# Kernel tuning notes

Measured on AMD Instinct MI355X. Metric: run time of the kernel, lower is better.

The kernel has to match this reference:

```python
import jax, jax.numpy as jnp
import numpy as np

V, D, H, L, F, S_MAX = 32000, 1024, 16, 4, 4096, 1024
DK = D // H
EPS = 1e-5


def pos_encoding(S, Dm):
    pos = jnp.arange(S, dtype=jnp.float32)[:, None]
    div = jnp.exp(jnp.arange(0, Dm, 2, dtype=jnp.float32) * (-jnp.log(10000.0) / Dm))
    ang = pos * div  # [S, D/2]
    return jnp.stack([jnp.sin(ang), jnp.cos(ang)], axis=-1).reshape(S, Dm)


def layernorm(x, g, b):
    mu = jnp.mean(x, axis=-1, keepdims=True)
    var = jnp.mean(jnp.square(x - mu), axis=-1, keepdims=True)
    return (x - mu) * jax.lax.rsqrt(var + EPS) * g + b


def setup_inputs() -> dict:
    key = jax.random.key(0)
    ks = jax.random.split(key, 20)
    s = 0.02
    B, S = 4, 1024
    x = jax.random.randint(ks[0], (B, S), 1, V)  # avoid pad token 0
    return {
        'x': x,
        'emb': jax.random.normal(ks[1], (V, D), jnp.float32) * s,
        'Wq': jax.random.normal(ks[2], (L, D, D), jnp.float32) * s,
        'Wk': jax.random.normal(ks[3], (L, D, D), jnp.float32) * s,
        'Wv': jax.random.normal(ks[4], (L, D, D), jnp.float32) * s,
        'Wo': jax.random.normal(ks[5], (L, D, D), jnp.float32) * s,
        'bo': jnp.zeros((L, D), jnp.float32),
        'ln1_g': jnp.ones((L, D), jnp.float32),
        'ln1_b': jnp.zeros((L, D), jnp.float32),
        'ln2_g': jnp.ones((L, D), jnp.float32),
        'ln2_b': jnp.zeros((L, D), jnp.float32),
        'W1': jax.random.normal(ks[6], (L, D, F), jnp.float32) * s,
        'b1': jnp.zeros((L, F), jnp.float32),
        'W2': jax.random.normal(ks[7], (L, F, D), jnp.float32) * s,
        'b2': jnp.zeros((L, D), jnp.float32),
        'Wout': jax.random.normal(ks[8], (D, V), jnp.float32) * s,
        'bout': jnp.zeros((V,), jnp.float32),
    }


def reference(x, emb, Wq, Wk, Wv, Wo, bo, ln1_g, ln1_b, ln2_g, ln2_b, W1, b1, W2, b2, Wout, bout):
    B, S = x.shape
    # mask: padding (key tokens != 0) AND causal, shape [B, 1, S, S]
    pad = (x != 0)[:, None, None, :]
    causal = jnp.tril(jnp.ones((S, S), bool))[None, None]
    mask = pad & causal

    h = emb[x] * jnp.sqrt(jnp.float32(D)) + pos_encoding(S, D)[None]

    scale = jnp.sqrt(jnp.float32(DK))
    for l in range(L):
        q = (h @ Wq[l]).reshape(B, S, H, DK).transpose(0, 2, 1, 3)
        k = (h @ Wk[l]).reshape(B, S, H, DK).transpose(0, 2, 1, 3)
        v = (h @ Wv[l]).reshape(B, S, H, DK).transpose(0, 2, 1, 3)
        scores = jnp.einsum('bhqd,bhkd->bhqk', q, k) / scale
        scores = jnp.where(mask, scores, -jnp.inf)
        attn = jax.nn.softmax(scores, axis=-1)
        ctx = jnp.einsum('bhqk,bhkd->bhqd', attn, v)
        ctx = ctx.transpose(0, 2, 1, 3).reshape(B, S, D)
        attn_out = ctx @ Wo[l] + bo[l]
        h = layernorm(h + attn_out, ln1_g[l], ln1_b[l])
        ff = jax.nn.gelu(h @ W1[l] + b1[l], approximate=False) @ W2[l] + b2[l]
        h = layernorm(h + ff, ln2_g[l], ln2_b[l])

    return h @ Wout + bout
```

## Files before the change

### kernel.cpp

```cpp
#include <hip/hip_runtime.h>
#include <hip/hip_bf16.h>
#include <math.h>

constexpr int Bc = 4, Sc = 1024, Dc = 1024, Hc = 16, Lc = 4, Fc = 4096, Vc = 32000;
constexpr int DKc = 64;
constexpr int Mc = Bc * Sc;
constexpr float EPSc = 1e-5f;

typedef __attribute__((ext_vector_type(8))) short short8v;
typedef __attribute__((ext_vector_type(4))) float f32x4;

__device__ __forceinline__ ushort bf16_rne(float f) {
    uint u = __float_as_uint(f);
    return (ushort)((u + 0x7fffu + ((u >> 16) & 1u)) >> 16);
}
__device__ __forceinline__ void split2(float f, ushort& h, ushort& l) {
    ushort hh = bf16_rne(f);
    float hf = __uint_as_float(((uint)hh) << 16);
    h = hh;
    l = bf16_rne(f - hf);
}

__global__ __launch_bounds__(256) void embed_k(const int* __restrict__ x,
                                               const float* __restrict__ emb,
                                               float* __restrict__ h) {
    int m = blockIdx.x;
    int s = m & (Sc - 1);
    int tid = threadIdx.x;
    int d0 = tid * 4;
    int tok = x[m];
    float4 e = *(const float4*)&emb[(size_t)tok * Dc + d0];
    const float c = -9.210340371976184f / 512.0f;
    float p0 = (float)(tid * 2);
    float fs = (float)s;
    float ang0 = fs * __expf(c * p0);
    float ang1 = fs * __expf(c * (p0 + 1.0f));
    float4 o;
    o.x = e.x * 32.0f + sinf(ang0);
    o.y = e.y * 32.0f + cosf(ang0);
    o.z = e.z * 32.0f + sinf(ang1);
    o.w = e.w * 32.0f + cosf(ang1);
    *(float4*)&h[(size_t)m * Dc + d0] = o;
}

__device__ __forceinline__ float gelu_exact(float v) {
    return 0.5f * v * (1.0f + erff(v * 0.70710678118654752f));
}

__global__ __launch_bounds__(256) void wconv_k(const float* __restrict__ W,
                                               ushort* __restrict__ hi,
                                               ushort* __restrict__ lo,
                                               int Kd, int Nd) {
    __shared__ float T[64][65];
    int nt = blockIdx.x * 64, kt = blockIdx.y * 64;
    int tid = threadIdx.x;
    int r16 = tid >> 4, c4 = (tid & 15) * 4;
#pragma unroll
    for (int p = 0; p < 4; p++) {
        int k = r16 + p * 16;
        float4 v = *(const float4*)&W[(size_t)(kt + k) * Nd + nt + c4];
        T[k][c4 + 0] = v.x; T[k][c4 + 1] = v.y;
        T[k][c4 + 2] = v.z; T[k][c4 + 3] = v.w;
    }
    __syncthreads();
#pragma unroll
    for (int p = 0; p < 4; p++) {
        int n = r16 + p * 16;
        ushort4 oh, ol;
        ushort hv, lv;
        split2(T[c4 + 0][n], hv, lv); oh.x = hv; ol.x = lv;
        split2(T[c4 + 1][n], hv, lv); oh.y = hv; ol.y = lv;
        split2(T[c4 + 2][n], hv, lv); oh.z = hv; ol.z = lv;
        split2(T[c4 + 3][n], hv, lv); oh.w = hv; ol.w = lv;
        size_t o = (size_t)(nt + n) * Kd + kt + c4;
        *(ushort4*)&hi[o] = oh;
        *(ushort4*)&lo[o] = ol;
    }
}

template<int MODE>
__global__ __launch_bounds__(256) void mgemm_k(const float* __restrict__ A,
                                               const ushort* __restrict__ Bh_g,
                                               const ushort* __restrict__ Bl_g,
                                               const float* __restrict__ bias,
                                               float* __restrict__ C,
                                               int Kd, int Nd) {
    __shared__ ushort Ah[128][40], Al[128][40], Bh[128][40], Bl[128][40];
    int tid = threadIdx.x;
    int bm = blockIdx.y * 128, bn = blockIdx.x * 128;
    int lane = tid & 63, w = tid >> 6;
    int wr = w >> 1, wc = w & 1;
    int l15 = lane & 15, loct = lane >> 4;

    int sr = tid >> 1, sh = tid & 1;
    const float*  Ap  = A    + (size_t)(bm + sr) * Kd + sh * 16;
    const ushort* Bhp = Bh_g + (size_t)(bn + sr) * Kd + sh * 16;
    const ushort* Blp = Bl_g + (size_t)(bn + sr) * Kd + sh * 16;

    f32x4 acc[4][4];
#pragma unroll
    for (int i = 0; i < 4; i++)
#pragma unroll
        for (int j = 0; j < 4; j++) acc[i][j] = (f32x4){0.f, 0.f, 0.f, 0.f};

    for (int k0 = 0; k0 < Kd; k0 += 32) {
        float4 a0 = *(const float4*)(Ap + k0 + 0);
        float4 a1 = *(const float4*)(Ap + k0 + 4);
        float4 a2 = *(const float4*)(Ap + k0 + 8);
        float4 a3 = *(const float4*)(Ap + k0 + 12);
        uint4 b0 = *(const uint4*)(Bhp + k0);
        uint4 b1 = *(const uint4*)(Bhp + k0 + 8);
        uint4 b2 = *(const uint4*)(Blp + k0);
        uint4 b3 = *(const uint4*)(Blp + k0 + 8);

        union { ushort u[16]; short8v v[2]; } hA, lA;
        float fa[16] = {a0.x, a0.y, a0.z, a0.w, a1.x, a1.y, a1.z, a1.w,
                        a2.x, a2.y, a2.z, a2.w, a3.x, a3.y, a3.z, a3.w};
#pragma unroll
        for (int i = 0; i < 16; i++) {
            ushort hv, lv;
            split2(fa[i], hv, lv);
            hA.u[i] = hv; lA.u[i] = lv;
        }

        __syncthreads();
        *(short8v*)&Ah[sr][sh * 16 + 0] = hA.v[0];
        *(short8v*)&Ah[sr][sh * 16 + 8] = hA.v[1];
        *(short8v*)&Al[sr][sh * 16 + 0] = lA.v[0];
        *(short8v*)&Al[sr][sh * 16 + 8] = lA.v[1];
        *(uint4*)&Bh[sr][sh * 16 + 0] = b0;
        *(uint4*)&Bh[sr][sh * 16 + 8] = b1;
        *(uint4*)&Bl[sr][sh * 16 + 0] = b2;
        *(uint4*)&Bl[sr][sh * 16 + 8] = b3;
        __syncthreads();

        short8v ah[4], al[4], bh[4], bl[4];
#pragma unroll
        for (int m = 0; m < 4; m++) {
            int r = wr * 64 + m * 16 + l15;
            ah[m] = *(const short8v*)&Ah[r][loct * 8];
            al[m] = *(const short8v*)&Al[r][loct * 8];
        }
#pragma unroll
        for (int n = 0; n < 4; n++) {
            int ccol = wc * 64 + n * 16 + l15;
            bh[n] = *(const short8v*)&Bh[ccol][loct * 8];
            bl[n] = *(const short8v*)&Bl[ccol][loct * 8];
        }
#pragma unroll
        for (int m = 0; m < 4; m++)
#pragma unroll
            for (int n = 0; n < 4; n++) {
                acc[m][n] = __builtin_amdgcn_mfma_f32_16x16x32_bf16(ah[m], bh[n], acc[m][n], 0, 0, 0);
                acc[m][n] = __builtin_amdgcn_mfma_f32_16x16x32_bf16(ah[m], bl[n], acc[m][n], 0, 0, 0);
                acc[m][n] = __builtin_amdgcn_mfma_f32_16x16x32_bf16(al[m], bh[n], acc[m][n], 0, 0, 0);
            }
    }

#pragma unroll
    for (int m = 0; m < 4; m++) {
#pragma unroll
        for (int n = 0; n < 4; n++) {
            int gn = bn + wc * 64 + n * 16 + l15;
            float bv = (MODE == 1 || MODE == 2) ? bias[gn] : 0.0f;
#pragma unroll
            for (int j = 0; j < 4; j++) {
                int gm = bm + wr * 64 + m * 16 + loct * 4 + j;
                float v = acc[m][n][j];
                if (MODE == 1 || MODE == 2) v += bv;
                if (MODE == 2) v = gelu_exact(v);
                if (MODE == 3) {
                    int b = gm >> 10, s = gm & 1023;
                    int hh = gn >> 6, dk = gn & 63;
                    C[(((size_t)(b * Hc + hh) * Sc) + s) * DKc + dk] = v;
                } else {
                    C[(size_t)gm * Nd + gn] = v;
                }
            }
        }
    }
}

template<int MODE>
__global__ __launch_bounds__(256) void gemm_k(const float* __restrict__ A,
                                              const float* __restrict__ Bm,
                                              const float* __restrict__ bias,
                                              float* __restrict__ C,
                                              int Kd, int Nd) {
    __shared__ float As[16][68];
    __shared__ float Bs[16][68];
    int tid = threadIdx.x;
    int bm = blockIdx.y * 64;
    int bn = blockIdx.x * 64;
    int tx = tid & 15;
    int ty = tid >> 4;
    float acc[4][4] = {};

    int arow = tid >> 2;
    int akq  = tid & 3;
    int bkrow = tid >> 4;
    int bn4   = tid & 15;

    const float* Aptr = A + (size_t)(bm + arow) * Kd + akq * 4;
    const float* Bptr = Bm + (size_t)bkrow * Nd + bn + bn4 * 4;

    for (int k0 = 0; k0 < Kd; k0 += 16) {
        float4 av = *(const float4*)(Aptr + k0);
        float4 bv = *(const float4*)(Bptr + (size_t)k0 * Nd);
        As[akq * 4 + 0][arow] = av.x;
        As[akq * 4 + 1][arow] = av.y;
        As[akq * 4 + 2][arow] = av.z;
        As[akq * 4 + 3][arow] = av.w;
        *(float4*)&Bs[bkrow][bn4 * 4] = bv;
        __syncthreads();
#pragma unroll
        for (int kk = 0; kk < 16; kk++) {
            float4 a4 = *(const float4*)&As[kk][ty * 4];
            float4 b4 = *(const float4*)&Bs[kk][tx * 4];
            acc[0][0] += a4.x * b4.x; acc[0][1] += a4.x * b4.y;
            acc[0][2] += a4.x * b4.z; acc[0][3] += a4.x * b4.w;
            acc[1][0] += a4.y * b4.x; acc[1][1] += a4.y * b4.y;
            acc[1][2] += a4.y * b4.z; acc[1][3] += a4.y * b4.w;
            acc[2][0] += a4.z * b4.x; acc[2][1] += a4.z * b4.y;
            acc[2][2] += a4.z * b4.z; acc[2][3] += a4.z * b4.w;
            acc[3][0] += a4.w * b4.x; acc[3][1] += a4.w * b4.y;
            acc[3][2] += a4.w * b4.z; acc[3][3] += a4.w * b4.w;
        }
        __syncthreads();
    }

#pragma unroll
    for (int i = 0; i < 4; i++) {
        int gm = bm + ty * 4 + i;
#pragma unroll
        for (int j = 0; j < 4; j++) {
            int gn = bn + tx * 4 + j;
            float v = acc[i][j];
            if (MODE == 1 || MODE == 2) v += bias[gn];
            if (MODE == 2) v = gelu_exact(v);
            C[(size_t)gm * Nd + gn] = v;
        }
    }
}

constexpr int QT = 64;
constexpr int KT = 32;

__global__ __launch_bounds__(64) void fattn_k(const float* __restrict__ Q,
                                              const float* __restrict__ K,
                                              const float* __restrict__ V,
                                              const int* __restrict__ x,
                                              float* __restrict__ ctx) {
    int qt = blockIdx.x;
    int bh = blockIdx.y;
    int b = bh >> 4;
    int hh = bh & 15;
    int tid = threadIdx.x;
    int q = qt * QT + tid;

    __shared__ float Ks[KT][64];
    __shared__ float Vs[KT][64];
    __shared__ int   xs[KT];

    const float* Kb = K + (size_t)bh * Sc * DKc;
    const float* Vb = V + (size_t)bh * Sc * DKc;

    float4 q4[16];
    const float* qp = Q + ((size_t)bh * Sc + q) * DKc;
#pragma unroll
    for (int i = 0; i < 16; i++) q4[i] = *(const float4*)(qp + 4 * i);

    float4 acc[16];
#pragma unroll
    for (int i = 0; i < 16; i++) acc[i] = make_float4(0.f, 0.f, 0.f, 0.f);
    float m = -INFINITY, l = 0.0f;

    int ktiles = (qt * QT + QT) / KT;
    for (int t = 0; t < ktiles; t++) {
        int k0 = t * KT;
        __syncthreads();
        for (int f = tid; f < KT * 16; f += 64) {
            int kr = f >> 4;
            int dc = (f & 15) * 4;
            *(float4*)&Ks[kr][dc] = *(const float4*)&Kb[(size_t)(k0 + kr) * DKc + dc];
            *(float4*)&Vs[kr][dc] = *(const float4*)&Vb[(size_t)(k0 + kr) * DKc + dc];
        }
        if (tid < KT) xs[tid] = x[b * Sc + k0 + tid];
        __syncthreads();

        float sc[KT];
#pragma unroll
        for (int k = 0; k < KT; k++) {
            float4 s4 = make_float4(0.f, 0.f, 0.f, 0.f);
#pragma unroll
            for (int i = 0; i < 16; i++) {
                float4 kv = *(const float4*)&Ks[k][4 * i];
                s4.x += q4[i].x * kv.x;
                s4.y += q4[i].y * kv.y;
                s4.z += q4[i].z * kv.z;
                s4.w += q4[i].w * kv.w;
            }
            float s = (s4.x + s4.y) + (s4.z + s4.w);
            bool valid = ((k0 + k) <= q) && (xs[k] != 0);
            sc[k] = valid ? s * 0.125f : -INFINITY;
        }

        float tm = sc[0];
#pragma unroll
        for (int k = 1; k < KT; k++) tm = fmaxf(tm, sc[k]);
        float mnew = fmaxf(m, tm);
        float corr = __expf(m - mnew);
        l *= corr;
#pragma unroll
        for (int i = 0; i < 16; i++) {
            acc[i].x *= corr; acc[i].y *= corr;
            acc[i].z *= corr; acc[i].w *= corr;
        }
        m = mnew;

#pragma unroll
        for (int k = 0; k < KT; k++) {
            float p = __expf(sc[k] - m);
            l += p;
#pragma unroll
            for (int i = 0; i < 16; i++) {
                float4 vv = *(const float4*)&Vs[k][4 * i];
                acc[i].x += p * vv.x;
                acc[i].y += p * vv.y;
                acc[i].z += p * vv.z;
                acc[i].w += p * vv.w;
            }
        }
    }

    float inv = 1.0f / l;
    float* op = ctx + ((size_t)b * Sc + q) * Dc + hh * 64;
#pragma unroll
    for (int i = 0; i < 16; i++) {
        float4 o;
        o.x = acc[i].x * inv; o.y = acc[i].y * inv;
        o.z = acc[i].z * inv; o.w = acc[i].w * inv;
        *(float4*)(op + 4 * i) = o;
    }
}

__global__ __launch_bounds__(256) void lnadd_k(const float* x, const float* r,
                                               const float* __restrict__ g,
                                               const float* __restrict__ bb,
                                               float* out) {
    int row = blockIdx.x, tid = threadIdx.x;
    int lane = tid & 63, wid = tid >> 6;
    __shared__ float red[8];
    size_t base = (size_t)row * Dc + tid * 4;
    float4 xv = *(const float4*)(x + base);
    float4 rv = *(const float4*)(r + base);
    float v0 = xv.x + rv.x, v1 = xv.y + rv.y, v2 = xv.z + rv.z, v3 = xv.w + rv.w;
    float sum = v0 + v1 + v2 + v3;
    float sq = v0 * v0 + v1 * v1 + v2 * v2 + v3 * v3;
    for (int off = 32; off; off >>= 1) {
        sum += __shfl_down(sum, off);
        sq  += __shfl_down(sq, off);
    }
    if (lane == 0) { red[wid] = sum; red[4 + wid] = sq; }
    __syncthreads();
    if (tid == 0) {
        red[0] = red[0] + red[1] + red[2] + red[3];
        red[4] = red[4] + red[5] + red[6] + red[7];
    }
    __syncthreads();
    float mu = red[0] * (1.0f / Dc);
    float var = red[4] * (1.0f / Dc) - mu * mu;
    float rs = rsqrtf(var + EPSc);
    int d = tid * 4;
    float4 gv = *(const float4*)(g + d);
    float4 bv = *(const float4*)(bb + d);
    float4 o;
    o.x = (v0 - mu) * rs * gv.x + bv.x;
    o.y = (v1 - mu) * rs * gv.y + bv.y;
    o.z = (v2 - mu) * rs * gv.z + bv.z;
    o.w = (v3 - mu) * rs * gv.w + bv.w;
    *(float4*)(out + base) = o;
}

extern "C" void kernel_launch(void* const* d_in, const int* in_sizes, int n_in,
                              void* d_out, int out_size, void* d_ws, size_t ws_size,
                              hipStream_t stream) {
    const int*   x     = (const int*)d_in[0];
    const float* emb   = (const float*)d_in[1];
    const float* Wq    = (const float*)d_in[2];
    const float* Wk    = (const float*)d_in[3];
    const float* Wv    = (const float*)d_in[4];
    const float* Wo    = (const float*)d_in[5];
    const float* bo    = (const float*)d_in[6];
    const float* ln1g  = (const float*)d_in[7];
    const float* ln1b  = (const float*)d_in[8];
    const float* ln2g  = (const float*)d_in[9];
    const float* ln2b  = (const float*)d_in[10];
    const float* W1    = (const float*)d_in[11];
    const float* b1    = (const float*)d_in[12];
    const float* W2    = (const float*)d_in[13];
    const float* b2    = (const float*)d_in[14];
    const float* Wout  = (const float*)d_in[15];
    const float* bout  = (const float*)d_in[16];
    float* out = (float*)d_out;
    float* ws = (float*)d_ws;

    const size_t MD = (size_t)Mc * Dc;
    float* h    = ws;
    float* q    = ws + 1 * MD;
    float* k    = ws + 2 * MD;
    float* v    = ws + 3 * MD;
    float* ctx  = ws + 4 * MD;
    float* tmp  = ws + 5 * MD;
    float* ff1  = q;

    const size_t DD = (size_t)Dc * Dc;
    const size_t DF = (size_t)Dc * Fc;
    const size_t PL = 8 * DD + 4 * DF;
    ushort* conv = (ushort*)out;

    const size_t used  = 6 * MD * sizeof(float);
    const size_t woutE = (size_t)Dc * Vc;
    bool wout_mfma = ws_size >= used + 2 * woutE * sizeof(ushort);
    ushort* woc_h = (ushort*)((char*)ws + used);
    ushort* woc_l = woc_h + woutE;

    embed_k<<<Mc, 256, 0, stream>>>(x, emb, h);

    for (int l = 0; l < Lc; l++) {
        ushort* base = conv + (size_t)l * PL;
        wconv_k<<<dim3(16, 16), 256, 0, stream>>>(Wq + (size_t)l * DD, base + 0 * DD, base + 1 * DD, Dc, Dc);
        wconv_k<<<dim3(16, 16), 256, 0, stream>>>(Wk + (size_t)l * DD, base + 2 * DD, base + 3 * DD, Dc, Dc);
        wconv_k<<<dim3(16, 16), 256, 0, stream>>>(Wv + (size_t)l * DD, base + 4 * DD, base + 5 * DD, Dc, Dc);
        wconv_k<<<dim3(16, 16), 256, 0, stream>>>(Wo + (size_t)l * DD, base + 6 * DD, base + 7 * DD, Dc, Dc);
        wconv_k<<<dim3(64, 16), 256, 0, stream>>>(W1 + (size_t)l * DF, base + 8 * DD, base + 8 * DD + DF, Dc, Fc);
        wconv_k<<<dim3(16, 64), 256, 0, stream>>>(W2 + (size_t)l * DF, base + 8 * DD + 2 * DF, base + 8 * DD + 3 * DF, Fc, Dc);
    }
    if (wout_mfma)
        wconv_k<<<dim3(Vc / 64, 16), 256, 0, stream>>>(Wout, woc_h, woc_l, Dc, Vc);

    dim3 g1(Dc / 128, Mc / 128);
    dim3 gF(Fc / 128, Mc / 128);
    dim3 gV(Vc / 128, Mc / 128);

    for (int l = 0; l < Lc; l++) {
        ushort* base = conv + (size_t)l * PL;

        mgemm_k<3><<<g1, 256, 0, stream>>>(h, base + 0 * DD, base + 1 * DD, nullptr, q, Dc, Dc);
        mgemm_k<3><<<g1, 256, 0, stream>>>(h, base + 2 * DD, base + 3 * DD, nullptr, k, Dc, Dc);
        mgemm_k<3><<<g1, 256, 0, stream>>>(h, base + 4 * DD, base + 5 * DD, nullptr, v, Dc, Dc);

        fattn_k<<<dim3(Sc / QT, Bc * Hc), QT, 0, stream>>>(q, k, v, x, ctx);

        mgemm_k<1><<<g1, 256, 0, stream>>>(ctx, base + 6 * DD, base + 7 * DD, bo + l * Dc, tmp, Dc, Dc);
        lnadd_k<<<Mc, 256, 0, stream>>>(h, tmp, ln1g + l * Dc, ln1b + l * Dc, h);

        mgemm_k<2><<<gF, 256, 0, stream>>>(h, base + 8 * DD, base + 8 * DD + DF, b1 + l * Fc, ff1, Dc, Fc);
        mgemm_k<1><<<g1, 256, 0, stream>>>(ff1, base + 8 * DD + 2 * DF, base + 8 * DD + 3 * DF, b2 + l * Dc, tmp, Fc, Dc);
        lnadd_k<<<Mc, 256, 0, stream>>>(h, tmp, ln2g + l * Dc, ln2b + l * Dc, h);
    }

    if (wout_mfma)
        mgemm_k<1><<<gV, 256, 0, stream>>>(h, woc_h, woc_l, bout, out, Dc, Vc);
    else
        gemm_k<1><<<dim3(Vc / 64, Mc / 64), 256, 0, stream>>>(h, Wout, bout, out, Dc, Vc);
}
```

Before: 9.336 ms.

## Split attention key range across four waves per block with LSE merge

The flash-attention kernel now launches 256 threads per query tile. Each of four waves processes a quarter of the key sequence, skipping slices entirely above the causal limit. Partial max/sum/accumulators are merged through shared memory with a log-sum-exp reduction before writing the output. This raises parallelism and occupancy for the scalar attention kernel, at the cost of extra shared memory, synchronisation, and idle waves for early query tiles.

```diff
diff --git a/kernel.cpp b/kernel.cpp
--- a/kernel.cpp
+++ b/kernel.cpp
@@ -243,27 +243,35 @@
     }
 }
 
-constexpr int QT = 64;
-constexpr int KT = 32;
-
-__global__ __launch_bounds__(64) void fattn_k(const float* __restrict__ Q,
-                                              const float* __restrict__ K,
-                                              const float* __restrict__ V,
-                                              const int* __restrict__ x,
-                                              float* __restrict__ ctx) {
+constexpr int QT  = 64;
+constexpr int KT  = 16;
+constexpr int NW  = 4;
+constexpr int KSL = Sc / NW;
+constexpr int KSTR = 68;
+
+__global__ __launch_bounds__(256) void fattn_k(const float* __restrict__ Q,
+                                               const float* __restrict__ K,
+                                               const float* __restrict__ V,
+                                               const int* __restrict__ x,
+                                               float* __restrict__ ctx) {
+    __shared__ float smem[NW][2 * KT * KSTR];
+    __shared__ float red_m[NW][QT], red_l[NW][QT];
+    __shared__ float invL[QT];
+    __shared__ int   xs_s[NW][KT];
+
     int qt = blockIdx.x;
     int bh = blockIdx.y;
     int b = bh >> 4;
     int hh = bh & 15;
     int tid = threadIdx.x;
-    int q = qt * QT + tid;
-
-    __shared__ float Ks[KT][64];
-    __shared__ float Vs[KT][64];
-    __shared__ int   xs[KT];
+    int lane = tid & 63, w = tid >> 6;
+    int q = qt * QT + lane;
+    int qmax = qt * QT + QT - 1;
 
     const float* Kb = K + (size_t)bh * Sc * DKc;
     const float* Vb = V + (size_t)bh * Sc * DKc;
+    float* Kw = &smem[w][0];
+    float* Vw = Kw + KT * KSTR;
 
     float4 q4[16];
     const float* qp = Q + ((size_t)bh * Sc + q) * DKc;
@@ -275,18 +283,23 @@
     for (int i = 0; i < 16; i++) acc[i] = make_float4(0.f, 0.f, 0.f, 0.f);
     float m = -INFINITY, l = 0.0f;
 
-    int ktiles = (qt * QT + QT) / KT;
-    for (int t = 0; t < ktiles; t++) {
-        int k0 = t * KT;
-        __syncthreads();
-        for (int f = tid; f < KT * 16; f += 64) {
-            int kr = f >> 4;
-            int dc = (f & 15) * 4;
-            *(float4*)&Ks[kr][dc] = *(const float4*)&Kb[(size_t)(k0 + kr) * DKc + dc];
-            *(float4*)&Vs[kr][dc] = *(const float4*)&Vb[(size_t)(k0 + kr) * DKc + dc];
-        }
-        if (tid < KT) xs[tid] = x[b * Sc + k0 + tid];
-        __syncthreads();
+    for (int t = 0; t < KSL / KT; t++) {
+        int k0 = w * KSL + t * KT;
+        bool active = (k0 <= qmax);
+        __syncthreads();
+        if (active) {
+#pragma unroll
+            for (int i = 0; i < 4; i++) {
+                int f = lane + 64 * i;
+                int kr = f >> 4;
+                int dc = (f & 15) * 4;
+                *(float4*)&Kw[kr * KSTR + dc] = *(const float4*)&Kb[(size_t)(k0 + kr) * DKc + dc];
+                *(float4*)&Vw[kr * KSTR + dc] = *(const float4*)&Vb[(size_t)(k0 + kr) * DKc + dc];
+            }
+            if (lane < KT) xs_s[w][lane] = x[b * Sc + k0 + lane];
+        }
+        __syncthreads();
+        if (!active) continue;
 
         float sc[KT];
 #pragma unroll
@@ -294,14 +307,14 @@
             float4 s4 = make_float4(0.f, 0.f, 0.f, 0.f);
 #pragma unroll
             for (int i = 0; i < 16; i++) {
-                float4 kv = *(const float4*)&Ks[k][4 * i];
+                float4 kv = *(const float4*)&Kw[k * KSTR + 4 * i];
                 s4.x += q4[i].x * kv.x;
                 s4.y += q4[i].y * kv.y;
                 s4.z += q4[i].z * kv.z;
                 s4.w += q4[i].w * kv.w;
             }
             float s = (s4.x + s4.y) + (s4.z + s4.w);
-            bool valid = ((k0 + k) <= q) && (xs[k] != 0);
+            bool valid = ((k0 + k) <= q) && (xs_s[w][k] != 0);
             sc[k] = valid ? s * 0.125f : -INFINITY;
         }
 
@@ -324,7 +337,7 @@
             l += p;
 #pragma unroll
             for (int i = 0; i < 16; i++) {
-                float4 vv = *(const float4*)&Vs[k][4 * i];
+                float4 vv = *(const float4*)&Vw[k * KSTR + 4 * i];
                 acc[i].x += p * vv.x;
                 acc[i].y += p * vv.y;
                 acc[i].z += p * vv.z;
@@ -333,14 +346,56 @@
         }
     }
 
-    float inv = 1.0f / l;
-    float* op = ctx + ((size_t)b * Sc + q) * Dc + hh * 64;
-#pragma unroll
-    for (int i = 0; i < 16; i++) {
+    red_m[w][lane] = m;
+    red_l[w][lane] = l;
+    __syncthreads();
+
+    float M = red_m[0][lane];
+#pragma unroll
+    for (int wv = 1; wv < NW; wv++) M = fmaxf(M, red_m[wv][lane]);
+    float L = 0.0f;
+#pragma unroll
+    for (int wv = 0; wv < NW; wv++)
+        L += red_l[wv][lane] * __expf(red_m[wv][lane] - M);
+    float fw = __expf(m - M);
+    if (w == 0) invL[lane] = 1.0f / L;
+
+    float* outb = &smem[0][0];
+    for (int wv = 0; wv < NW; wv++) {
+        if (wv == w) {
+#pragma unroll
+            for (int i = 0; i < 16; i++) {
+                int d = 4 * i;
+                float vx = acc[i].x * fw, vy = acc[i].y * fw;
+                float vz = acc[i].z * fw, vw2 = acc[i].w * fw;
+                if (wv == 0) {
+                    outb[lane * 65 + d + 0] = vx;
+                    outb[lane * 65 + d + 1] = vy;
+                    outb[lane * 65 + d + 2] = vz;
+                    outb[lane * 65 + d + 3] = vw2;
+                } else {
+                    outb[lane * 65 + d + 0] += vx;
+                    outb[lane * 65 + d + 1] += vy;
+                    outb[lane * 65 + d + 2] += vz;
+                    outb[lane * 65 + d + 3] += vw2;
+                }
+            }
+        }
+        __syncthreads();
+    }
+
+    int qq = tid >> 2;
+    int d0 = (tid & 3) * 16;
+    float il = invL[qq];
+    float* op = ctx + ((size_t)b * Sc + qt * QT + qq) * Dc + hh * 64 + d0;
+#pragma unroll
+    for (int j = 0; j < 16; j += 4) {
         float4 o;
-        o.x = acc[i].x * inv; o.y = acc[i].y * inv;
-        o.z = acc[i].z * inv; o.w = acc[i].w * inv;
-        *(float4*)(op + 4 * i) = o;
+        o.x = outb[qq * 65 + d0 + j + 0] * il;
+        o.y = outb[qq * 65 + d0 + j + 1] * il;
+        o.z = outb[qq * 65 + d0 + j + 2] * il;
+        o.w = outb[qq * 65 + d0 + j + 3] * il;
+        *(float4*)(op + j) = o;
     }
 }
 
@@ -450,7 +505,7 @@
         mgemm_k<3><<<g1, 256, 0, stream>>>(h, base + 2 * DD, base + 3 * DD, nullptr, k, Dc, Dc);
         mgemm_k<3><<<g1, 256, 0, stream>>>(h, base + 4 * DD, base + 5 * DD, nullptr, v, Dc, Dc);
 
-        fattn_k<<<dim3(Sc / QT, Bc * Hc), QT, 0, stream>>>(q, k, v, x, ctx);
+        fattn_k<<<dim3(Sc / QT, Bc * Hc), 256, 0, stream>>>(q, k, v, x, ctx);
 
         mgemm_k<1><<<g1, 256, 0, stream>>>(ctx, base + 6 * DD, base + 7 * DD, bo + l * Dc, tmp, Dc, Dc);
         lnadd_k<<<Mc, 256, 0, stream>>>(h, tmp, ln1g + l * Dc, ln1b + l * Dc, h);
```

New measurement: 24.40 ms. +161.4%, slower.
